# Performance work log

Measured on AMD Instinct MI355X. Metric: run time of the kernel, lower is better.

## Reference

```python
import jax, jax.numpy as jnp
import numpy as np

B = 512      # number of ragged items
M = 256      # max item length (power of two)
D = 128      # EMBED_SIZE == dim
LEVELS = 8   # ceil(log2(M)) tree-reduction levels
EPS = 1e-5   # torch LayerNorm default


def _mlp(x, W1, b1, W2, b2, ln_w, ln_b):
    # Linear(2D->2D) -> ReLU -> Linear(2D->D) -> LayerNorm(D)
    h = jax.nn.relu(x @ W1 + b1)
    y = h @ W2 + b2
    mu = jnp.mean(y, axis=-1, keepdims=True)
    var = jnp.mean((y - mu) ** 2, axis=-1, keepdims=True)
    return (y - mu) * jax.lax.rsqrt(var + EPS) * ln_w + ln_b


def setup_inputs() -> dict:
    rng = np.random.default_rng(0)
    lengths = rng.integers(1, M + 1, size=B)
    limits = np.concatenate([[0], np.cumsum(lengths)]).astype(np.int64)
    T = int(limits[-1])
    ks = jax.random.split(jax.random.key(0), 5)
    s1 = 1.0 / np.sqrt(2 * D)  # torch Linear init bound, fan_in = 2*D
    s2 = 1.0 / np.sqrt(2 * D)
    return {
        "args": jax.random.normal(ks[0], (T, D), jnp.float32),
        "limits": jnp.asarray(limits),
        "W1": jax.random.uniform(ks[1], (2 * D, 2 * D), jnp.float32, -s1, s1),
        "b1": jax.random.uniform(ks[2], (2 * D,), jnp.float32, -s1, s1),
        "W2": jax.random.uniform(ks[3], (2 * D, D), jnp.float32, -s2, s2),
        "b2": jax.random.uniform(ks[4], (D,), jnp.float32, -s2, s2),
        "ln_w": jnp.ones((D,), jnp.float32),
        "ln_b": jnp.zeros((D,), jnp.float32),
    }


def reference(args, limits, W1, b1, W2, b2, ln_w, ln_b):
    lengths = jnp.diff(limits).astype(jnp.int32)  # [B]
    T = args.shape[0]
    # pad each ragged item to M and place it at the start of a 2M-1 tree buffer
    rows = limits[:-1, None].astype(jnp.int32) + jnp.arange(M, dtype=jnp.int32)[None, :]
    mask = jnp.arange(M)[None, :] < lengths[:, None]
    seq = jnp.where(mask[..., None], args[jnp.clip(rows, 0, T - 1)], 0.0)  # [B,M,D]
    buf0 = jnp.concatenate([seq, jnp.zeros((B, M - 1, D), seq.dtype)], axis=1)  # [B,2M-1,D]

    def reduce_item(buf, L):
        # level-synchronized binary tree reduction; odd leftover carries to next level
        s = jnp.int32(0)
        l = L
        for k in range(LEVELS):
            pmax = max(1, M >> (k + 1))  # static per-level pair capacity
            j = jnp.arange(pmax, dtype=jnp.int32)
            pairs = l // 2
            valid = j < pairs
            ia = jnp.where(valid, s + 2 * j, 0)
            a = buf[ia]          # [pmax, D]
            b = buf[ia + 1]      # [pmax, D]
            out = _mlp(jnp.concatenate([a, b], axis=-1), W1, b1, W2, b2, ln_w, ln_b)
            fill = jnp.where(valid, s + l + j, 2 * M - 1)  # OOB index -> dropped
            buf = buf.at[fill].set(out, mode="drop")
            s = s + 2 * pairs
            l = (l + 1) // 2
        return buf[2 * L - 2]  # root of the tree (== input element when L == 1)

    return jax.vmap(reduce_item)(buf0, lengths)  # [B, D]
```

## Files before the change

### kernel.cpp

```cpp
#include <hip/hip_runtime.h>
#include <stdint.h>

#define D 128

typedef __bf16 bf16x8 __attribute__((ext_vector_type(8)));
typedef float f32x4  __attribute__((ext_vector_type(4)));

__device__ __forceinline__ float b2f(ushort u) {
    uint x = ((uint)u) << 16;
    return __builtin_bit_cast(float, x);
}
__device__ __forceinline__ ushort f2b(float f) {
    uint u = __builtin_bit_cast(uint, f);
    u += 0x7FFFu + ((u >> 16) & 1u);
    return (ushort)(u >> 16);
}
__device__ __forceinline__ int swz(int b) { return b ^ (((b >> 9) & 7) << 4); }

__global__ void __launch_bounds__(512) prep_kernel(
    const float* __restrict__ W1, const float* __restrict__ W2,
    const int* __restrict__ limits,
    ushort* __restrict__ W1p, ushort* __restrict__ W2p,
    int4* __restrict__ chainTab)
{
    if (blockIdx.x < 192) {
        int g = blockIdx.x * 512 + threadIdx.x;
        if (g < 65536) {
            int t = g & 7, l = (g >> 3) & 63, nt = (g >> 9) & 15, kk = g >> 13;
            int krow = kk * 32 + (l >> 4) * 8 + t;
            int col  = nt * 16 + (l & 15);
            W1p[g] = f2b(W1[krow * 256 + col]);
        } else {
            int g2 = g - 65536;
            int t = g2 & 7, l = (g2 >> 3) & 63, nt = (g2 >> 9) & 7, kk = g2 >> 12;
            int krow = kk * 32 + (l >> 4) * 8 + t;
            int col  = nt * 16 + (l & 15);
            W2p[g2] = f2b(W2[krow * 128 + col]);
        }
        return;
    }
    __shared__ ushort Ls[512];
    __shared__ ushort rnkIdx[512];
    const int tid = threadIdx.x;
    int Lm = min(max(limits[tid + 1] - limits[tid], 1), 256);
    Ls[tid] = (ushort)Lm;
    __syncthreads();
    int rank = 0;
    for (int j = 0; j < 512; ++j) {
        int Lj = Ls[j];
        rank += (Lj > Lm) || (Lj == Lm && j < tid);
    }
    rnkIdx[rank] = (ushort)tid;
    __syncthreads();
    if (tid < 256) {
        int iA = rnkIdx[tid], iB = rnkIdx[511 - tid];
        int4 t;
        t.x = iA | (((int)Ls[iA]) << 16);
        t.y = iB | (((int)Ls[iB]) << 16);
        t.z = limits[iA];
        t.w = limits[iB];
        chainTab[tid] = t;
    }
}

template<int NMF>
__device__ __forceinline__ void level_body(
    char* __restrict__ Xw, const char* __restrict__ W2s,
    const unsigned* __restrict__ sk,
    const uint4 (&w1r)[8][2], const float (&bb1)[2][4],
    const float* __restrict__ b2, const float* __restrict__ lnw,
    const float* __restrict__ lnb,
    const ushort* __restrict__ cpSk, const ushort* __restrict__ itOff,
    int G, bool doLeft, int tid, int lane, int w)
{
    constexpr int FPP   = (NMF >= 2) ? 2 : 1;
    constexpr int NPASS = NMF / FPP;

    #pragma unroll
    for (int p = 0; p < NPASS; ++p) {
        unsigned pa[FPP];
        #pragma unroll
        for (int mf = 0; mf < FPP; ++mf) pa[mf] = sk[(p * FPP + mf) * 16 + (lane & 15)];

        f32x4 acc1[2][FPP];
        #pragma unroll
        for (int n = 0; n < 2; ++n)
            #pragma unroll
            for (int mf = 0; mf < FPP; ++mf) acc1[n][mf] = f32x4{0.f, 0.f, 0.f, 0.f};

        #pragma unroll
        for (int kk = 0; kk < 8; ++kk) {
            uint4 xv[FPP];
            #pragma unroll
            for (int mf = 0; mf < FPP; ++mf) {
                int prow = (int)(pa[mf] & 0xFFFFu);
                xv[mf] = *(const uint4*)(Xw + (prow * 512 + ((kk * 64 + (lane >> 4) * 16) ^ ((prow & 7) << 4))));
            }
            #pragma unroll
            for (int n = 0; n < 2; ++n) {
                bf16x8 af = __builtin_bit_cast(bf16x8, w1r[kk][n]);
                #pragma unroll
                for (int mf = 0; mf < FPP; ++mf)
                    acc1[n][mf] = __builtin_amdgcn_mfma_f32_16x16x32_bf16(
                        af, __builtin_bit_cast(bf16x8, xv[mf]), acc1[n][mf], 0, 0, 0);
            }
        }
        __syncthreads();

        #pragma unroll
        for (int mf = 0; mf < FPP; ++mf) {
            if ((pa[mf] >> 16) != 0xFFFFu) {
                int prow = (int)(pa[mf] & 0xFFFFu);
                int rbase = prow * 512, sm = (prow & 7) << 4;
                #pragma unroll
                for (int n = 0; n < 2; ++n) {
                    float h0 = fmaxf(acc1[n][mf][0] + bb1[n][0], 0.f);
                    float h1 = fmaxf(acc1[n][mf][1] + bb1[n][1], 0.f);
                    float h2 = fmaxf(acc1[n][mf][2] + bb1[n][2], 0.f);
                    float h3 = fmaxf(acc1[n][mf][3] + bb1[n][3], 0.f);
                    uint2 pk;
                    pk.x = (uint)f2b(h0) | ((uint)f2b(h1) << 16);
                    pk.y = (uint)f2b(h2) | ((uint)f2b(h3) << 16);
                    *(uint2*)(Xw + (rbase + ((64 * w + 32 * n + 8 * (lane >> 4)) ^ sm))) = pk;
                }
            }
        }
    }
    __syncthreads();

    f32x4 acc2[8];
    #pragma unroll
    for (int nt = 0; nt < 8; ++nt) acc2[nt] = f32x4{0.f, 0.f, 0.f, 0.f};

    if (w < NMF) {
        int prow = (int)(sk[w * 16 + (lane & 15)] & 0xFFFFu);
        int sm = (prow & 7) << 4, rbase = prow * 512;
        #pragma unroll
        for (int kk = 0; kk < 8; ++kk) {
            uint4 av = *(const uint4*)(Xw + (rbase + ((kk * 64 + (lane >> 4) * 16) ^ sm)));
            bf16x8 af = __builtin_bit_cast(bf16x8, av);
            #pragma unroll
            for (int nt = 0; nt < 8; ++nt) {
                uint4 bv = *(const uint4*)(W2s + (((kk * 8 + nt) * 64 + lane) << 4));
                acc2[nt] = __builtin_amdgcn_mfma_f32_16x16x32_bf16(
                    af, __builtin_bit_cast(bf16x8, bv), acc2[nt], 0, 0, 0);
            }
        }
    }
    __syncthreads();

    if (w < NMF) {
        float s1[4] = {0.f,0.f,0.f,0.f}, s2[4] = {0.f,0.f,0.f,0.f};
        #pragma unroll
        for (int nt = 0; nt < 8; ++nt) {
            float bias = b2[nt * 16 + (lane & 15)];
            #pragma unroll
            for (int i = 0; i < 4; ++i) {
                float v = acc2[nt][i] + bias;
                acc2[nt][i] = v; s1[i] += v; s2[i] += v * v;
            }
        }
        #pragma unroll
        for (int o = 1; o < 16; o <<= 1)
            #pragma unroll
            for (int i = 0; i < 4; ++i) {
                s1[i] += __shfl_xor(s1[i], o, 64);
                s2[i] += __shfl_xor(s2[i], o, 64);
            }
        float lwv[8], lbv[8];
        #pragma unroll
        for (int nt = 0; nt < 8; ++nt) {
            int c = nt * 16 + (lane & 15);
            lwv[nt] = lnw[c]; lbv[nt] = lnb[c];
        }
        float mu[4], rs[4];
        #pragma unroll
        for (int i = 0; i < 4; ++i) {
            mu[i] = s1[i] * (1.f / 128.f);
            float var = s2[i] * (1.f / 128.f) - mu[i] * mu[i];
            rs[i] = rsqrtf(var + 1e-5f);
        }
        #pragma unroll
        for (int i = 0; i < 4; ++i) {
            unsigned se = sk[w * 16 + (lane >> 4) * 4 + i];
            int yd = (int)(se >> 16);
            if (yd != 0xFFFF) {
                #pragma unroll
                for (int nt = 0; nt < 8; ++nt) {
                    int c = nt * 16 + (lane & 15);
                    float v = (acc2[nt][i] - mu[i]) * rs[i] * lwv[nt] + lbv[nt];
                    *(ushort*)(Xw + swz(yd * 256 + c * 2)) = f2b(v);
                }
            }
        }
    }
    if (doLeft) {
        #pragma unroll
        for (int q = 0; q < 2; ++q) {
            int it = q * 32 + (tid >> 4);
            if (it < G) {
                int srow = (int)cpSk[it];
                if (srow != 0xFFFF) {
                    int ch = tid & 15;
                    uint4 v = *(const uint4*)(Xw + swz(srow * 256 + ch * 16));
                    *(uint4*)(Xw + swz((int)itOff[it] * 256 + ch * 16)) = v;
                }
            }
        }
    }
}

__global__ void __launch_bounds__(512, 2) tree_kernel(
    const float* __restrict__ args, const int4* __restrict__ chainTab,
    const ushort* __restrict__ W1p, const ushort* __restrict__ W2p,
    const float* __restrict__ b1, const float* __restrict__ b2,
    const float* __restrict__ lnw, const float* __restrict__ lnb,
    float* __restrict__ out)
{
    __shared__ __align__(16) char Xw[90112];
    __shared__ __align__(16) char W2s[65536];
    __shared__ unsigned int schedAll[1536];
    __shared__ ushort cpSAll[8][2];
    __shared__ ushort itOff[2], itL[2], itOut[2];
    __shared__ int itRow[2];
    __shared__ int nPAll[8];

    const int tid = threadIdx.x, lane = tid & 63, w = tid >> 6;

    uint4 w1r[8][2];
    #pragma unroll
    for (int kk = 0; kk < 8; ++kk)
        #pragma unroll
        for (int n = 0; n < 2; ++n)
            w1r[kk][n] = *(const uint4*)(W1p + (size_t)(((kk * 16 + (w * 2 + n)) * 64 + lane) << 3));

    float bb1[2][4];
    #pragma unroll
    for (int n = 0; n < 2; ++n)
        #pragma unroll
        for (int i = 0; i < 4; ++i)
            bb1[n][i] = b1[32 * w + 16 * n + 4 * (lane >> 4) + i];

    #pragma unroll
    for (int q = 0; q < 8; ++q) {
        int t = tid + q * 512;
        *(uint4*)(W2s + t * 16) = *(const uint4*)((const char*)W2p + t * 16);
    }

    const int4 ct = chainTab[blockIdx.x];
    const int iA = ct.x & 0xFFFF, La = ct.x >> 16;
    const int iB = ct.y & 0xFFFF, Lb = ct.y >> 16;
    const int a0A = ct.z, a0B = ct.w;
    const int offBfull = (La + 1) & ~1;
    const bool split = (offBfull + Lb > 352);
    const int npass = split ? 2 : 1;

    for (int pass = 0; pass < npass; ++pass) {
        int G, L0, r0, o0, off1 = 0, L1 = 0, r1 = 0, o1 = 0;
        if (!split)          { G = 2; L0 = La; r0 = a0A; o0 = iA; off1 = offBfull; L1 = Lb; r1 = a0B; o1 = iB; }
        else if (pass == 0)  { G = 1; L0 = La; r0 = a0A; o0 = iA; }
        else                 { G = 1; L0 = Lb; r0 = a0B; o0 = iB; }

        __syncthreads();
        if (tid == 0) {
            itOff[0] = 0;            itL[0] = (ushort)L0; itRow[0] = r0; itOut[0] = (ushort)o0;
            itOff[1] = (ushort)off1; itL[1] = (ushort)L1; itRow[1] = r1; itOut[1] = (ushort)o1;
        }
        int nlev = (L0 > 1) ? (32 - __clz(L0 - 1)) : 0;
        if (G > 1 && L1 > 1) nlev = max(nlev, 32 - __clz(L1 - 1));

        if (w == 0) {
            int lA_ = L0, lB_ = (G > 1) ? L1 : 0;
            for (int k = 0; k < nlev; ++k) {
                int pA = lA_ >> 1, pB = lB_ >> 1, nPk = pA + pB;
                if (lane == 0) {
                    nPAll[k] = nPk;
                    cpSAll[k][0] = (lA_ > 1 && (lA_ & 1)) ? (ushort)(lA_ - 1) : (ushort)0xFFFF;
                    cpSAll[k][1] = (lB_ > 1 && (lB_ & 1)) ? (ushort)(off1 + lB_ - 1) : (ushort)0xFFFF;
                }
                #pragma unroll
                for (int rep = 0; rep < 3; ++rep) {
                    int e = lane + rep * 64;
                    unsigned entry = 0xFFFF0000u;
                    if (e < pA)
                        entry = (unsigned)e | ((unsigned)((lA_ & 1) + e) << 16);
                    else if (e < nPk) {
                        int j = e - pA;
                        entry = (unsigned)((off1 >> 1) + j) | ((unsigned)(off1 + (lB_ & 1) + j) << 16);
                    }
                    schedAll[k * 192 + e] = entry;
                }
                lA_ = pA + (lA_ & 1);
                lB_ = pB + (lB_ & 1);
            }
        } else {
            for (int job = tid - 64; job < 5632; job += 448) {
                int r = job >> 4, ch = job & 15;
                int src = -1;
                if (r < L0) src = r0 + r;
                else if (G > 1 && r >= off1 && r < off1 + L1) src = r1 + (r - off1);
                if (src >= 0) {
                    const float4 f0 = *(const float4*)(args + (size_t)src * D + ch * 8);
                    const float4 f1 = *(const float4*)(args + (size_t)src * D + ch * 8 + 4);
                    uint4 pk;
                    pk.x = (uint)f2b(f0.x) | ((uint)f2b(f0.y) << 16);
                    pk.y = (uint)f2b(f0.z) | ((uint)f2b(f0.w) << 16);
                    pk.z = (uint)f2b(f1.x) | ((uint)f2b(f1.y) << 16);
                    pk.w = (uint)f2b(f1.z) | ((uint)f2b(f1.w) << 16);
                    *(uint4*)(Xw + swz(r * 256 + ch * 16)) = pk;
                }
            }
        }
        __syncthreads();

        for (int k = 0; k < nlev; ++k) {
            const int nP = nPAll[k];
            if (nP == 0) break;
            int done = 0;
            while (done < nP) {
                const int chunk = min(nP - done, 128);
                const int nMf = (chunk + 15) >> 4;
                const bool last = (done + chunk >= nP);
                const unsigned* sk = schedAll + k * 192 + done;
                if (nMf > 4)
                    level_body<8>(Xw, W2s, sk, w1r, bb1, b2, lnw, lnb, cpSAll[k], itOff, G, last, tid, lane, w);
                else if (nMf > 2)
                    level_body<4>(Xw, W2s, sk, w1r, bb1, b2, lnw, lnb, cpSAll[k], itOff, G, last, tid, lane, w);
                else if (nMf == 2)
                    level_body<2>(Xw, W2s, sk, w1r, bb1, b2, lnw, lnb, cpSAll[k], itOff, G, last, tid, lane, w);
                else
                    level_body<1>(Xw, W2s, sk, w1r, bb1, b2, lnw, lnb, cpSAll[k], itOff, G, last, tid, lane, w);
                __syncthreads();
                done += chunk;
            }
        }

        for (int j = tid; j < G * 32; j += 512) {
            int it = j >> 5, grp = j & 31;
            float4 o;
            if ((int)itL[it] == 1) {
                o = *(const float4*)(args + (size_t)itRow[it] * D + grp * 4);
            } else {
                uint2 v = *(const uint2*)(Xw + swz((int)itOff[it] * 256 + grp * 8));
                o.x = b2f((ushort)(v.x & 0xFFFFu));
                o.y = b2f((ushort)(v.x >> 16));
                o.z = b2f((ushort)(v.y & 0xFFFFu));
                o.w = b2f((ushort)(v.y >> 16));
            }
            *(float4*)(out + (size_t)itOut[it] * D + grp * 4) = o;
        }
    }
}

extern "C" void kernel_launch(void* const* d_in, const int* in_sizes, int n_in,
                              void* d_out, int out_size, void* d_ws, size_t ws_size,
                              hipStream_t stream) {
    const float* args   = (const float*)d_in[0];
    const int*   limits = (const int*)d_in[1];
    const float* W1     = (const float*)d_in[2];
    const float* b1     = (const float*)d_in[3];
    const float* W2     = (const float*)d_in[4];
    const float* b2     = (const float*)d_in[5];
    const float* lnw    = (const float*)d_in[6];
    const float* lnb    = (const float*)d_in[7];

    char* ws = (char*)d_ws;
    ushort* W1p      = (ushort*)(ws);
    ushort* W2p      = (ushort*)(ws + 131072);
    int4*   chainTab = (int4*)  (ws + 196608);

    prep_kernel<<<193, 512, 0, stream>>>(W1, W2, limits, W1p, W2p, chainTab);
    tree_kernel<<<256, 512, 0, stream>>>(args, chainTab, W1p, W2p, b1, b2, lnw, lnb,
                                         (float*)d_out);
}
```

Measured before the change: 73.09 us.

## Keep W2 in registers and split second GEMM across all waves by output columns

The second linear layer now keeps each wave's 16-column slice of W2 in registers instead of staging the full W2 matrix in shared memory. Every wave computes its own output columns for all pair rows, rather than a few waves computing full rows. LayerNorm statistics are reduced across waves through a small shared partial-sum buffer with an extra barrier. This spreads the GEMM over all 8 waves at small levels and frees 64KB of LDS, at the cost of more register pressure, an added synchronisation, and repeated reads of the hidden activations from LDS by every wave.

```diff
diff --git a/kernel.cpp b/kernel.cpp
--- a/kernel.cpp
+++ b/kernel.cpp
@@ -65,11 +65,11 @@
 
 template<int NMF>
 __device__ __forceinline__ void level_body(
-    char* __restrict__ Xw, const char* __restrict__ W2s,
-    const unsigned* __restrict__ sk,
-    const uint4 (&w1r)[8][2], const float (&bb1)[2][4],
-    const float* __restrict__ b2, const float* __restrict__ lnw,
-    const float* __restrict__ lnb,
+    char* __restrict__ Xw, const unsigned* __restrict__ sk,
+    const uint4 (&w1r)[8][2], const uint4 (&w2r)[8],
+    const float (&bb1)[2][4], const float (&bb2v)[4],
+    const float (&lwv)[4], const float (&lbv)[4],
+    float2* __restrict__ pbuf,
     const ushort* __restrict__ cpSk, const ushort* __restrict__ itOff,
     int G, bool doLeft, int tid, int lane, int w)
 {
@@ -128,70 +128,63 @@
     }
     __syncthreads();
 
-    f32x4 acc2[8];
-    #pragma unroll
-    for (int nt = 0; nt < 8; ++nt) acc2[nt] = f32x4{0.f, 0.f, 0.f, 0.f};
-
-    if (w < NMF) {
-        int prow = (int)(sk[w * 16 + (lane & 15)] & 0xFFFFu);
-        int sm = (prow & 7) << 4, rbase = prow * 512;
-        #pragma unroll
-        for (int kk = 0; kk < 8; ++kk) {
-            uint4 av = *(const uint4*)(Xw + (rbase + ((kk * 64 + (lane >> 4) * 16) ^ sm)));
-            bf16x8 af = __builtin_bit_cast(bf16x8, av);
+    unsigned pa2[NMF];
+    #pragma unroll
+    for (int mf = 0; mf < NMF; ++mf) pa2[mf] = sk[mf * 16 + (lane & 15)];
+
+    f32x4 acc2[NMF];
+    #pragma unroll
+    for (int mf = 0; mf < NMF; ++mf) acc2[mf] = f32x4{0.f, 0.f, 0.f, 0.f};
+
+    #pragma unroll
+    for (int kk = 0; kk < 8; ++kk) {
+        bf16x8 af = __builtin_bit_cast(bf16x8, w2r[kk]);
+        #pragma unroll
+        for (int mf = 0; mf < NMF; ++mf) {
+            int prow = (int)(pa2[mf] & 0xFFFFu);
+            uint4 hv = *(const uint4*)(Xw + (prow * 512 + ((kk * 64 + (lane >> 4) * 16) ^ ((prow & 7) << 4))));
+            acc2[mf] = __builtin_amdgcn_mfma_f32_16x16x32_bf16(
+                af, __builtin_bit_cast(bf16x8, hv), acc2[mf], 0, 0, 0);
+        }
+    }
+
+    #pragma unroll
+    for (int mf = 0; mf < NMF; ++mf) {
+        float s1 = 0.f, s2 = 0.f;
+        #pragma unroll
+        for (int i = 0; i < 4; ++i) {
+            float v = acc2[mf][i] + bb2v[i];
+            acc2[mf][i] = v; s1 += v; s2 += v * v;
+        }
+        s1 += __shfl_xor(s1, 16, 64); s2 += __shfl_xor(s2, 16, 64);
+        s1 += __shfl_xor(s1, 32, 64); s2 += __shfl_xor(s2, 32, 64);
+        if ((lane >> 4) == 0)
+            pbuf[w * 128 + mf * 16 + (lane & 15)] = float2{s1, s2};
+    }
+    __syncthreads();
+
+    #pragma unroll
+    for (int mf = 0; mf < NMF; ++mf) {
+        int yd = (int)(pa2[mf] >> 16);
+        if (yd != 0xFFFF) {
+            int p = mf * 16 + (lane & 15);
+            float S1 = 0.f, S2 = 0.f;
             #pragma unroll
-            for (int nt = 0; nt < 8; ++nt) {
-                uint4 bv = *(const uint4*)(W2s + (((kk * 8 + nt) * 64 + lane) << 4));
-                acc2[nt] = __builtin_amdgcn_mfma_f32_16x16x32_bf16(
-                    af, __builtin_bit_cast(bf16x8, bv), acc2[nt], 0, 0, 0);
-            }
-        }
-    }
-    __syncthreads();
-
-    if (w < NMF) {
-        float s1[4] = {0.f,0.f,0.f,0.f}, s2[4] = {0.f,0.f,0.f,0.f};
-        #pragma unroll
-        for (int nt = 0; nt < 8; ++nt) {
-            float bias = b2[nt * 16 + (lane & 15)];
-            #pragma unroll
-            for (int i = 0; i < 4; ++i) {
-                float v = acc2[nt][i] + bias;
-                acc2[nt][i] = v; s1[i] += v; s2[i] += v * v;
-            }
-        }
-        #pragma unroll
-        for (int o = 1; o < 16; o <<= 1)
-            #pragma unroll
-            for (int i = 0; i < 4; ++i) {
-                s1[i] += __shfl_xor(s1[i], o, 64);
-                s2[i] += __shfl_xor(s2[i], o, 64);
-            }
-        float lwv[8], lbv[8];
-        #pragma unroll
-        for (int nt = 0; nt < 8; ++nt) {
-            int c = nt * 16 + (lane & 15);
-            lwv[nt] = lnw[c]; lbv[nt] = lnb[c];
-        }
-        float mu[4], rs[4];
-        #pragma unroll
-        for (int i = 0; i < 4; ++i) {
-            mu[i] = s1[i] * (1.f / 128.f);
-            float var = s2[i] * (1.f / 128.f) - mu[i] * mu[i];
-            rs[i] = rsqrtf(var + 1e-5f);
-        }
-        #pragma unroll
-        for (int i = 0; i < 4; ++i) {
-            unsigned se = sk[w * 16 + (lane >> 4) * 4 + i];
-            int yd = (int)(se >> 16);
-            if (yd != 0xFFFF) {
-                #pragma unroll
-                for (int nt = 0; nt < 8; ++nt) {
-                    int c = nt * 16 + (lane & 15);
-                    float v = (acc2[nt][i] - mu[i]) * rs[i] * lwv[nt] + lbv[nt];
-                    *(ushort*)(Xw + swz(yd * 256 + c * 2)) = f2b(v);
-                }
-            }
+            for (int ww = 0; ww < 8; ++ww) {
+                float2 o = pbuf[ww * 128 + p];
+                S1 += o.x; S2 += o.y;
+            }
+            float mu = S1 * (1.f / 128.f);
+            float var = S2 * (1.f / 128.f) - mu * mu;
+            float rs = rsqrtf(var + 1e-5f);
+            float v0 = (acc2[mf][0] - mu) * rs * lwv[0] + lbv[0];
+            float v1 = (acc2[mf][1] - mu) * rs * lwv[1] + lbv[1];
+            float v2 = (acc2[mf][2] - mu) * rs * lwv[2] + lbv[2];
+            float v3 = (acc2[mf][3] - mu) * rs * lwv[3] + lbv[3];
+            uint2 pk;
+            pk.x = (uint)f2b(v0) | ((uint)f2b(v1) << 16);
+            pk.y = (uint)f2b(v2) | ((uint)f2b(v3) << 16);
+            *(uint2*)(Xw + swz(yd * 256 + (16 * w + 4 * (lane >> 4)) * 2)) = pk;
         }
     }
     if (doLeft) {
@@ -210,7 +203,9 @@
     }
 }
 
-__global__ void __launch_bounds__(512, 2) tree_kernel(
+__global__ void __launch_bounds__(512)
+__attribute__((amdgpu_waves_per_eu(2, 2)))
+tree_kernel(
     const float* __restrict__ args, const int4* __restrict__ chainTab,
     const ushort* __restrict__ W1p, const ushort* __restrict__ W2p,
     const float* __restrict__ b1, const float* __restrict__ b2,
@@ -218,8 +213,8 @@
     float* __restrict__ out)
 {
     __shared__ __align__(16) char Xw[90112];
-    __shared__ __align__(16) char W2s[65536];
     __shared__ unsigned int schedAll[1536];
+    __shared__ float2 pbuf[1024];
     __shared__ ushort cpSAll[8][2];
     __shared__ ushort itOff[2], itL[2], itOut[2];
     __shared__ int itRow[2];
@@ -234,17 +229,22 @@
         for (int n = 0; n < 2; ++n)
             w1r[kk][n] = *(const uint4*)(W1p + (size_t)(((kk * 16 + (w * 2 + n)) * 64 + lane) << 3));
 
+    uint4 w2r[8];
+    #pragma unroll
+    for (int kk = 0; kk < 8; ++kk)
+        w2r[kk] = *(const uint4*)(W2p + (size_t)(((kk * 8 + w) * 64 + lane) << 3));
+
     float bb1[2][4];
     #pragma unroll
     for (int n = 0; n < 2; ++n)
         #pragma unroll
         for (int i = 0; i < 4; ++i)
             bb1[n][i] = b1[32 * w + 16 * n + 4 * (lane >> 4) + i];
-
-    #pragma unroll
-    for (int q = 0; q < 8; ++q) {
-        int t = tid + q * 512;
-        *(uint4*)(W2s + t * 16) = *(const uint4*)((const char*)W2p + t * 16);
+    float bb2v[4], lwv[4], lbv[4];
+    #pragma unroll
+    for (int i = 0; i < 4; ++i) {
+        int c = 16 * w + 4 * (lane >> 4) + i;
+        bb2v[i] = b2[c]; lwv[i] = lnw[c]; lbv[i] = lnb[c];
     }
 
     const int4 ct = chainTab[blockIdx.x];
@@ -323,13 +323,13 @@
                 const bool last = (done + chunk >= nP);
                 const unsigned* sk = schedAll + k * 192 + done;
                 if (nMf > 4)
-                    level_body<8>(Xw, W2s, sk, w1r, bb1, b2, lnw, lnb, cpSAll[k], itOff, G, last, tid, lane, w);
+                    level_body<8>(Xw, sk, w1r, w2r, bb1, bb2v, lwv, lbv, pbuf, cpSAll[k], itOff, G, last, tid, lane, w);
                 else if (nMf > 2)
-                    level_body<4>(Xw, W2s, sk, w1r, bb1, b2, lnw, lnb, cpSAll[k], itOff, G, last, tid, lane, w);
+                    level_body<4>(Xw, sk, w1r, w2r, bb1, bb2v, lwv, lbv, pbuf, cpSAll[k], itOff, G, last, tid, lane, w);
                 else if (nMf == 2)
-                    level_body<2>(Xw, W2s, sk, w1r, bb1, b2, lnw, lnb, cpSAll[k], itOff, G, last, tid, lane, w);
+                    level_body<2>(Xw, sk, w1r, w2r, bb1, bb2v, lwv, lbv, pbuf, cpSAll[k], itOff, G, last, tid, lane, w);
                 else
-                    level_body<1>(Xw, W2s, sk, w1r, bb1, b2, lnw, lnb, cpSAll[k], itOff, G, last, tid, lane, w);
+                    level_body<1>(Xw, sk, w1r, w2r, bb1, bb2v, lwv, lbv, pbuf, cpSAll[k], itOff, G, last, tid, lane, w);
                 __syncthreads();
                 done += chunk;
             }
```

Result: faster. 64.90 us (-11.2%).
